# Performance work log

Hardware: AMD Instinct MI355X
Metric: run time of the kernel (lower is better)

The kernel has to match this reference:

```python
import jax, jax.numpy as jnp
import numpy as np


def setup_inputs() -> dict:
    key = jax.random.key(0)
    k0, k1, k2, k3, k4 = jax.random.split(key, 5)
    B, d_inner, L, d_state = 64, 384, 197, 16
    x = jax.random.normal(k0, (B, d_inner, L), dtype=jnp.float32)
    # deltaA = exp(delta*A) lies in (0,1); uniform keeps the recurrence stable
    deltaA = jax.random.uniform(k1, (B, d_inner, L, d_state), dtype=jnp.float32)
    deltaB = jax.random.normal(k2, (B, d_inner, L, d_state), dtype=jnp.float32)
    C = jax.random.normal(k3, (B, d_state, L), dtype=jnp.float32)
    D = jax.random.normal(k4, (d_inner,), dtype=jnp.float32)
    return {"x": x, "deltaA": deltaA, "deltaB": deltaB, "C": C, "D": D}


def reference(x, deltaA, deltaB, C, D):
    """Selective scan: h_t = deltaB_t*x_t + deltaA_t*h_{t-1}; y_t = h_t @ C_t.
    x:(B,d,L) deltaA/deltaB:(B,d,L,n) C:(B,n,L) D:(d,)
    """
    deltaB_x = deltaB * x[..., None]              # (B,d,L,n)
    dA_t = jnp.moveaxis(deltaA, 2, 0)             # (L,B,d,n)
    dBx_t = jnp.moveaxis(deltaB_x, 2, 0)          # (L,B,d,n)
    C_t = jnp.moveaxis(C, 2, 0)                   # (L,B,n)

    def step(h, inputs):
        a, bx, c = inputs
        h = bx + a * h                            # (B,d,n)
        y = jnp.einsum("bdn,bn->bd", h, c)        # (B,d)
        return h, y

    h0 = jnp.zeros(dA_t.shape[1:], dtype=x.dtype)
    _, ys = jax.lax.scan(step, h0, (dA_t, dBx_t, C_t))  # ys: (L,B,d)
    y = jnp.moveaxis(ys, 0, 2)                    # (B,d,L)
    return y + x * D[:, None]
```

## Files before the change

kernel.cpp:

```cpp
#include <hip/hip_runtime.h>


#define B_   64
#define DIN  384
#define L_   197
#define N_   16
#define GROUPS_PER_BLOCK 16

__global__ __launch_bounds__(256)
void ssm_scan_kernel(const float* __restrict__ x,
                     const float* __restrict__ dA,
                     const float* __restrict__ dB,
                     const float* __restrict__ C,
                     const float* __restrict__ D,
                     float* __restrict__ y)
{
    __shared__ float Cs[N_ * L_];

    const int tid = threadIdx.x;
    const int b   = blockIdx.y;

    const float* Cg = C + (size_t)b * (N_ * L_);
    for (int i = tid; i < N_ * L_; i += 256) Cs[i] = Cg[i];
    __syncthreads();

    const int grp = tid >> 4;
    const int n   = tid & 15;
    const int d   = blockIdx.x * GROUPS_PER_BLOCK + grp;

    const size_t bd = (size_t)b * DIN + d;
    const float* pA = dA + bd * (size_t)(L_ * N_) + n;
    const float* pB = dB + bd * (size_t)(L_ * N_) + n;
    const float* px = x  + bd * L_;
    float*       py = y  + bd * L_;
    const float  Dd = D[d];
    const float* Cn = Cs + n * L_;

    float h = 0.0f;
    int t = 0;

    for (; t + 4 <= L_; t += 4) {
        const float a0 = pA[(t+0)*N_], a1 = pA[(t+1)*N_];
        const float a2 = pA[(t+2)*N_], a3 = pA[(t+3)*N_];
        const float g0 = pB[(t+0)*N_], g1 = pB[(t+1)*N_];
        const float g2 = pB[(t+2)*N_], g3 = pB[(t+3)*N_];
        const float x0 = px[t+0], x1 = px[t+1], x2 = px[t+2], x3 = px[t+3];
        const float c0 = Cn[t+0], c1 = Cn[t+1], c2 = Cn[t+2], c3 = Cn[t+3];

        h = fmaf(a0, h, g0 * x0);  float p0 = h * c0;
        h = fmaf(a1, h, g1 * x1);  float p1 = h * c1;
        h = fmaf(a2, h, g2 * x2);  float p2 = h * c2;
        h = fmaf(a3, h, g3 * x3);  float p3 = h * c3;

        #pragma unroll
        for (int m = 1; m < 16; m <<= 1) {
            p0 += __shfl_xor(p0, m);
            p1 += __shfl_xor(p1, m);
            p2 += __shfl_xor(p2, m);
            p3 += __shfl_xor(p3, m);
        }

        if (n == 0) {
            py[t+0] = fmaf(x0, Dd, p0);
            py[t+1] = fmaf(x1, Dd, p1);
            py[t+2] = fmaf(x2, Dd, p2);
            py[t+3] = fmaf(x3, Dd, p3);
        }
    }

    for (; t < L_; ++t) {
        const float a  = pA[t*N_];
        const float g  = pB[t*N_];
        const float xv = px[t];
        h = fmaf(a, h, g * xv);
        float p = h * Cn[t];
        #pragma unroll
        for (int m = 1; m < 16; m <<= 1) p += __shfl_xor(p, m);
        if (n == 0) py[t] = fmaf(xv, Dd, p);
    }
}

extern "C" void kernel_launch(void* const* d_in, const int* in_sizes, int n_in,
                              void* d_out, int out_size, void* d_ws, size_t ws_size,
                              hipStream_t stream) {
    const float* x  = (const float*)d_in[0];
    const float* dA = (const float*)d_in[1];
    const float* dB = (const float*)d_in[2];
    const float* C  = (const float*)d_in[3];
    const float* D  = (const float*)d_in[4];
    float* y = (float*)d_out;

    dim3 grid(DIN / GROUPS_PER_BLOCK, B_);
    dim3 block(256);
    ssm_scan_kernel<<<grid, block, 0, stream>>>(x, dA, dB, C, D, y);
}
```

Measured before the change: 162.8 us.

## Rewrite scan with async global-to-LDS double-buffered staging and DPP reductions

Replaces the 256-thread kernel, which used one thread per state element, with a 64-thread kernel where each thread holds four state elements. dA, dB and x tiles of eight timesteps are streamed into LDS through global_load_lds and double-buffered, with manual vmcnt waits. C is transposed into LDS so it can be read as float4, and the cross-lane reduction uses two DPP adds instead of four shuffles. The intent is to hide memory latency and cut shuffle and load overhead. The cost is fewer waves per CU, since each block is a single wave, and fragile hand-written waitcnt and tail handling.

```diff
diff --git a/kernel.cpp b/kernel.cpp
--- a/kernel.cpp
+++ b/kernel.cpp
@@ -1,83 +1,121 @@
 #include <hip/hip_runtime.h>
 
 
-#define B_   64
-#define DIN  384
-#define L_   197
-#define N_   16
-#define GROUPS_PER_BLOCK 16
+#define B_    64
+#define DIN   384
+#define L_    197
+#define N_    16
+#define TS    8
+#define NFULL 24
+#define T0TAIL 189
 
-__global__ __launch_bounds__(256)
-void ssm_scan_kernel(const float* __restrict__ x,
-                     const float* __restrict__ dA,
-                     const float* __restrict__ dB,
-                     const float* __restrict__ C,
-                     const float* __restrict__ D,
-                     float* __restrict__ y)
+#define BUFW  4352
+#define BWB   2112
+#define XW    4224
+#define CSW   8704
+#define LDSW  (CSW + L_*N_)
+
+typedef unsigned int u32as1 __attribute__((address_space(1)));
+typedef unsigned int u32as3 __attribute__((address_space(3)));
+
+__device__ __forceinline__ void gll16(const float* g, float* l) {
+    __builtin_amdgcn_global_load_lds((const u32as1*)g, (u32as3*)l, 16, 0, 0);
+}
+__device__ __forceinline__ void gll4(const float* g, float* l) {
+    __builtin_amdgcn_global_load_lds((const u32as1*)g, (u32as3*)l, 4, 0, 0);
+}
+
+#define DPPADD(p, C) do { \
+    int _r = __builtin_amdgcn_update_dpp(0, __float_as_int(p), (C), 0xF, 0xF, true); \
+    (p) += __int_as_float(_r); } while (0)
+
+__device__ __forceinline__ void stage_tile(const float* sA, const float* sB,
+                                           const float* sX, float* ab, int t0) {
+#pragma unroll
+    for (int p = 0; p < 8; ++p) gll16(sA + p * (2 * L_ * N_) + t0 * N_, ab + p * 264);
+#pragma unroll
+    for (int p = 0; p < 8; ++p) gll16(sB + p * (2 * L_ * N_) + t0 * N_, ab + BWB + p * 264);
+    gll4(sX + t0 + 0, ab + XW + 0);
+    gll4(sX + t0 + 4, ab + XW + 64);
+}
+
+__global__ __launch_bounds__(64, 1)
+void ssm_dma(const float* __restrict__ x, const float* __restrict__ dA,
+             const float* __restrict__ dB, const float* __restrict__ C,
+             const float* __restrict__ D, float* __restrict__ y)
 {
-    __shared__ float Cs[N_ * L_];
+    __shared__ __align__(16) float lds[LDSW];
 
     const int tid = threadIdx.x;
     const int b   = blockIdx.y;
+    const int d0  = blockIdx.x * 16;
+    const int g   = tid >> 2;
+    const int q   = tid & 3;
 
     const float* Cg = C + (size_t)b * (N_ * L_);
-    for (int i = tid; i < N_ * L_; i += 256) Cs[i] = Cg[i];
+    for (int i = tid; i < N_ * L_; i += 64) {
+        const int n = i / L_;
+        const int t = i - n * L_;
+        lds[CSW + t * N_ + n] = Cg[i];
+    }
     __syncthreads();
 
-    const int grp = tid >> 4;
-    const int n   = tid & 15;
-    const int d   = blockIdx.x * GROUPS_PER_BLOCK + grp;
+    const int bd0 = b * DIN + d0;
+    const float* sA = dA + (size_t)(bd0 + (tid >> 5)) * (L_ * N_) + (tid & 31) * 4;
+    const float* sB = dB + (size_t)(bd0 + (tid >> 5)) * (L_ * N_) + (tid & 31) * 4;
+    const float* sX = x  + (size_t)(bd0 + g) * L_ + q;
+    float*      pyL = y  + (size_t)(bd0 + g) * L_;
+    const float  Dd = D[d0 + g];
 
-    const size_t bd = (size_t)b * DIN + d;
-    const float* pA = dA + bd * (size_t)(L_ * N_) + n;
-    const float* pB = dB + bd * (size_t)(L_ * N_) + n;
-    const float* px = x  + bd * L_;
-    float*       py = y  + bd * L_;
-    const float  Dd = D[d];
-    const float* Cn = Cs + n * L_;
+    const int abL = (g >> 1) * 264 + (g & 1) * 128 + q * 4;
+    const int csL = CSW + q * 4;
+    const int xL  = XW + g * 4;
 
-    float h = 0.0f;
-    int t = 0;
+    float h0 = 0.f, h1 = 0.f, h2 = 0.f, h3 = 0.f, ya = 0.f, yb = 0.f;
 
-    for (; t + 4 <= L_; t += 4) {
-        const float a0 = pA[(t+0)*N_], a1 = pA[(t+1)*N_];
-        const float a2 = pA[(t+2)*N_], a3 = pA[(t+3)*N_];
-        const float g0 = pB[(t+0)*N_], g1 = pB[(t+1)*N_];
-        const float g2 = pB[(t+2)*N_], g3 = pB[(t+3)*N_];
-        const float x0 = px[t+0], x1 = px[t+1], x2 = px[t+2], x3 = px[t+3];
-        const float c0 = Cn[t+0], c1 = Cn[t+1], c2 = Cn[t+2], c3 = Cn[t+3];
+#define STEP(li, ABB, CSB, XB) do { \
+    const float4 a4 = *(const float4*)(lds + (ABB) + (li) * 16); \
+    const float4 g4 = *(const float4*)(lds + (ABB) + BWB + (li) * 16); \
+    const float4 c4 = *(const float4*)(lds + (CSB) + (li) * 16); \
+    const float xv  = lds[(XB) + ((li) >> 2) * 64 + ((li) & 3)]; \
+    h0 = fmaf(a4.x, h0, g4.x * xv); \
+    h1 = fmaf(a4.y, h1, g4.y * xv); \
+    h2 = fmaf(a4.z, h2, g4.z * xv); \
+    h3 = fmaf(a4.w, h3, g4.w * xv); \
+    float p = fmaf(h0, c4.x, fmaf(h1, c4.y, fmaf(h2, c4.z, h3 * c4.w))); \
+    DPPADD(p, 0xB1); \
+    DPPADD(p, 0x4E); \
+    const float yt = fmaf(xv, Dd, p); \
+    if (((li) & 3) == q) { if ((li) < 4) ya = yt; else yb = yt; } \
+} while (0)
 
-        h = fmaf(a0, h, g0 * x0);  float p0 = h * c0;
-        h = fmaf(a1, h, g1 * x1);  float p1 = h * c1;
-        h = fmaf(a2, h, g2 * x2);  float p2 = h * c2;
-        h = fmaf(a3, h, g3 * x3);  float p3 = h * c3;
-
-        #pragma unroll
-        for (int m = 1; m < 16; m <<= 1) {
-            p0 += __shfl_xor(p0, m);
-            p1 += __shfl_xor(p1, m);
-            p2 += __shfl_xor(p2, m);
-            p3 += __shfl_xor(p3, m);
-        }
-
-        if (n == 0) {
-            py[t+0] = fmaf(x0, Dd, p0);
-            py[t+1] = fmaf(x1, Dd, p1);
-            py[t+2] = fmaf(x2, Dd, p2);
-            py[t+3] = fmaf(x3, Dd, p3);
-        }
+    stage_tile(sA, sB, sX, lds, 0);
+    for (int k = 0; k < NFULL; ++k) {
+        const int tn = (k + 1 < NFULL) ? (k + 1) * TS : T0TAIL;
+        stage_tile(sA, sB, sX, lds + ((k + 1) & 1) * BUFW, tn);
+        asm volatile("s_waitcnt vmcnt(18)" ::: "memory");
+        const int ABB = (k & 1) * BUFW + abL;
+        const int CSB = csL + k * TS * N_;
+        const int XB  = (k & 1) * BUFW + xL;
+        const int t0  = k * TS;
+        STEP(0, ABB, CSB, XB); STEP(1, ABB, CSB, XB);
+        STEP(2, ABB, CSB, XB); STEP(3, ABB, CSB, XB);
+        STEP(4, ABB, CSB, XB); STEP(5, ABB, CSB, XB);
+        STEP(6, ABB, CSB, XB); STEP(7, ABB, CSB, XB);
+        pyL[t0 + q]     = ya;
+        pyL[t0 + 4 + q] = yb;
     }
-
-    for (; t < L_; ++t) {
-        const float a  = pA[t*N_];
-        const float g  = pB[t*N_];
-        const float xv = px[t];
-        h = fmaf(a, h, g * xv);
-        float p = h * Cn[t];
-        #pragma unroll
-        for (int m = 1; m < 16; m <<= 1) p += __shfl_xor(p, m);
-        if (n == 0) py[t] = fmaf(xv, Dd, p);
+    asm volatile("s_waitcnt vmcnt(0)" ::: "memory");
+    {
+        const int ABB = abL;
+        const int CSB = csL + T0TAIL * N_;
+        const int XB  = xL;
+        STEP(3, ABB, CSB, XB); STEP(4, ABB, CSB, XB); STEP(5, ABB, CSB, XB);
+        STEP(6, ABB, CSB, XB); STEP(7, ABB, CSB, XB);
+        if (q == 3) pyL[192] = ya;
+        pyL[193 + q] = yb;
     }
+#undef STEP
 }
 
 extern "C" void kernel_launch(void* const* d_in, const int* in_sizes, int n_in,
@@ -90,7 +128,7 @@
     const float* D  = (const float*)d_in[4];
     float* y = (float*)d_out;
 
-    dim3 grid(DIN / GROUPS_PER_BLOCK, B_);
-    dim3 block(256);
-    ssm_scan_kernel<<<grid, block, 0, stream>>>(x, dA, dB, C, D, y);
+    dim3 grid(DIN / 16, B_);
+    dim3 block(64);
+    ssm_dma<<<grid, block, 0, stream>>>(x, dA, dB, C, D, y);
 }
```

After: 149.0 us. -8.5%, faster.
